# Optimization experiments

Measured on AMD Instinct MI355X. Metric: run time of the kernel, lower is better.

The kernel has to match this reference:

```python
import jax, jax.numpy as jnp
import numpy as np

N_NODES = 50000
N_EDGES = 800000
F_IN = 16
F_OUT = 16
HID = 256


def _glorot(key, shape):
    fan_in, fan_out = shape[0], shape[1]
    lim = np.sqrt(6.0 / (fan_in + fan_out)).astype(np.float32)
    return jax.random.uniform(key, shape, jnp.float32, -lim, lim)


def setup_inputs() -> dict:
    key = jax.random.key(0)
    ks = jax.random.split(key, 12)
    x = jax.random.normal(ks[0], (N_NODES, F_IN), jnp.float32)
    edge_index = jax.random.randint(ks[1], (2, N_EDGES), 0, N_NODES, jnp.int64 if jax.config.jax_enable_x64 else jnp.int32)
    return {
        "x": x,
        "edge_index": edge_index,
        # mlp_pre: Linear(F_IN,HID) -> ReLU -> Linear(HID,HID)
        "pre_w1": _glorot(ks[2], (F_IN, HID)),
        "pre_b1": jnp.zeros((HID,), jnp.float32),
        "pre_w2": _glorot(ks[3], (HID, HID)),
        "pre_b2": jnp.zeros((HID,), jnp.float32),
        # GNCAConv edge transform: W h_j + b
        "conv_w": _glorot(ks[4], (HID, HID)),
        "conv_b": jnp.zeros((HID,), jnp.float32),
        # mlp_post: Linear(2*HID,HID) -> ReLU -> Linear(HID,F_OUT)
        "post_w1": _glorot(ks[5], (2 * HID, HID)),
        "post_b1": jnp.zeros((HID,), jnp.float32),
        "post_w2": _glorot(ks[6], (HID, F_OUT)),
        "post_b2": jnp.zeros((F_OUT,), jnp.float32),
    }


def reference(x, edge_index, pre_w1, pre_b1, pre_w2, pre_b2,
              conv_w, conv_b, post_w1, post_b1, post_w2, post_b2):
    # 1. pre-processing MLP: h_i = MLP_pre(s_i)
    h = jax.nn.relu(x @ pre_w1 + pre_b1) @ pre_w2 + pre_b2  # (N, HID)

    # 2. message passing: h_i || sum_{j in N(i)} ReLU(W h_j + b)
    src, dst = edge_index[0], edge_index[1]
    msg = jax.nn.relu(h[src] @ conv_w + conv_b)  # (E, HID)
    agg = jax.ops.segment_sum(msg, dst, num_segments=h.shape[0])  # (N, HID)
    h = jnp.concatenate([h, agg], axis=-1)  # (N, 2*HID)

    # 3. post-processing MLP + tanh output activation
    out = jax.nn.relu(h @ post_w1 + post_b1) @ post_w2 + post_b2
    return jnp.tanh(out)
```

## Files before the change

kernel.cpp:

```cpp
#include <hip/hip_runtime.h>
#include <hip/hip_bf16.h>

using f16x8 = __attribute__((ext_vector_type(8))) _Float16;
using f32x4 = __attribute__((ext_vector_type(4))) float;
using u16 = unsigned short;

__device__ __forceinline__ u16 f2h(float v) {
    _Float16 h = (_Float16)v;
    u16 r; __builtin_memcpy(&r, &h, 2); return r;
}
__device__ __forceinline__ float h2f(u16 x) {
    _Float16 h; __builtin_memcpy(&h, &x, 2); return (float)h;
}

__device__ __forceinline__ int fsw(int row) { return (row & 3) ^ ((row >> 2) & 3); }
__device__ __forceinline__ int aoff(int row, int kq) {
    return row * 32 + ((kq ^ fsw(row)) * 8);
}

__device__ __forceinline__ void gl16(const u16* g, const u16* l) {
    __builtin_amdgcn_global_load_lds(
        (const __attribute__((address_space(1))) unsigned int*)g,
        (__attribute__((address_space(3))) unsigned int*)l, 16, 0, 0);
}

template<int ACT>
__global__ __launch_bounds__(512, 4)
void mfma_k(const u16* __restrict__ A, int lda,
            const u16* __restrict__ BT,
            const float* __restrict__ bias,
            u16* __restrict__ Ch,
            int ldc, int M, int K) {
    __shared__ u16 As[2][128 * 32];
    __shared__ u16 Bs[2][256 * 32];

    const int tid  = threadIdx.x;
    const int brow = blockIdx.x * 128;
    const int lane = tid & 63;
    const int w    = tid >> 6;
    const int wr = w >> 2, wc = w & 3;
    const int lr = lane & 15, lq = lane >> 4;

    const int rsub = lane >> 2;
    const int s    = lane & 3;
    const int rowA  = w * 16 + rsub;
    const int rowB0 = w * 16 + rsub;
    const int rowB1 = 128 + w * 16 + rsub;
    const u16* gA  = A  + (size_t)(brow + rowA) * lda + (s ^ fsw(rowA))  * 8;
    const u16* gB0 = BT + (size_t)rowB0        * K   + (s ^ fsw(rowB0)) * 8;
    const u16* gB1 = BT + (size_t)rowB1        * K   + (s ^ fsw(rowB1)) * 8;

    f32x4 acc[4][4] = {};

#define STAGE(buf, koff)                                                       \
    do {                                                                       \
        gl16(gA  + (koff), &As[buf][w * 512]);                                 \
        gl16(gB0 + (koff), &Bs[buf][w * 512]);                                 \
        gl16(gB1 + (koff), &Bs[buf][(8 + w) * 512]);                           \
    } while (0)

    STAGE(0, 0);
    __syncthreads();

    const int nt = K >> 5;
    int cur = 0;
    for (int t = 0; t < nt; ++t) {
        if (t + 1 < nt) STAGE(cur ^ 1, (t + 1) * 32);

        f16x8 bf[4];
        #pragma unroll
        for (int n = 0; n < 4; ++n)
            bf[n] = *reinterpret_cast<const f16x8*>(&Bs[cur][aoff(wc * 64 + n * 16 + lr, lq)]);
        #pragma unroll
        for (int m = 0; m < 4; ++m) {
            f16x8 af = *reinterpret_cast<const f16x8*>(&As[cur][aoff(wr * 64 + m * 16 + lr, lq)]);
            #pragma unroll
            for (int n = 0; n < 4; ++n)
                acc[m][n] = __builtin_amdgcn_mfma_f32_16x16x32_f16(af, bf[n], acc[m][n], 0, 0, 0);
        }

        if (t + 1 < nt) {
            __syncthreads();
            cur ^= 1;
        }
    }
#undef STAGE

    #pragma unroll
    for (int m = 0; m < 4; ++m) {
        #pragma unroll
        for (int n = 0; n < 4; ++n) {
            #pragma unroll
            for (int r = 0; r < 4; ++r) {
                int grow = brow + wr * 64 + m * 16 + lq * 4 + r;
                if (grow >= M) continue;
                int gcol = wc * 64 + n * 16 + lr;
                float v = acc[m][n][r] + bias[gcol];
                if (ACT == 1) v = fmaxf(v, 0.f);
                Ch[(size_t)grow * ldc + gcol] = f2h(v);
            }
        }
    }
}

__global__ __launch_bounds__(512, 4)
void mfmaz_k(const u16* __restrict__ A, int lda,
             const u16* __restrict__ BT,
             const float* __restrict__ bias,
             const u16* __restrict__ P2T, const float* __restrict__ b2,
             float* __restrict__ out, int M, int K) {
    __shared__ u16 pool[2 * 128 * 32 + 2 * 256 * 32];
    u16 (*As)[128 * 32] = reinterpret_cast<u16(*)[128 * 32]>(pool);
    u16 (*Bs)[256 * 32] = reinterpret_cast<u16(*)[256 * 32]>(pool + 2 * 128 * 32);
    u16 (*zs)[136]      = reinterpret_cast<u16(*)[136]>(pool);

    const int tid  = threadIdx.x;
    const int brow = blockIdx.x * 128;
    const int lane = tid & 63;
    const int w    = tid >> 6;
    const int wr = w >> 2, wc = w & 3;
    const int lr = lane & 15, lq = lane >> 4;

    const int rsub = lane >> 2;
    const int s    = lane & 3;
    const int rowA  = w * 16 + rsub;
    const int rowB0 = w * 16 + rsub;
    const int rowB1 = 128 + w * 16 + rsub;
    const u16* gA  = A  + (size_t)(brow + rowA) * lda + (s ^ fsw(rowA))  * 8;
    const u16* gB0 = BT + (size_t)rowB0        * K   + (s ^ fsw(rowB0)) * 8;
    const u16* gB1 = BT + (size_t)rowB1        * K   + (s ^ fsw(rowB1)) * 8;

    f32x4 acc[4][4] = {};

#define STAGE(buf, koff)                                                       \
    do {                                                                       \
        gl16(gA  + (koff), &As[buf][w * 512]);                                 \
        gl16(gB0 + (koff), &Bs[buf][w * 512]);                                 \
        gl16(gB1 + (koff), &Bs[buf][(8 + w) * 512]);                           \
    } while (0)

    STAGE(0, 0);
    __syncthreads();

    const int nt = K >> 5;
    int cur = 0;
    for (int t = 0; t < nt; ++t) {
        if (t + 1 < nt) STAGE(cur ^ 1, (t + 1) * 32);

        f16x8 bf[4];
        #pragma unroll
        for (int n = 0; n < 4; ++n)
            bf[n] = *reinterpret_cast<const f16x8*>(&Bs[cur][aoff(wc * 64 + n * 16 + lr, lq)]);
        #pragma unroll
        for (int m = 0; m < 4; ++m) {
            f16x8 af = *reinterpret_cast<const f16x8*>(&As[cur][aoff(wr * 64 + m * 16 + lr, lq)]);
            #pragma unroll
            for (int n = 0; n < 4; ++n)
                acc[m][n] = __builtin_amdgcn_mfma_f32_16x16x32_f16(af, bf[n], acc[m][n], 0, 0, 0);
        }

        if (t + 1 < nt) {
            __syncthreads();
            cur ^= 1;
        }
    }
#undef STAGE

    __syncthreads();

    f32x4 acc2 = {};
    #pragma unroll
    for (int p = 0; p < 2; ++p) {
        if ((wc >> 1) == p) {
            const int colp = (wc & 1) * 64;
            #pragma unroll
            for (int m = 0; m < 4; ++m) {
                #pragma unroll
                for (int n = 0; n < 4; ++n) {
                    #pragma unroll
                    for (int r = 0; r < 4; ++r) {
                        int row  = wr * 64 + m * 16 + lq * 4 + r;
                        int gcol = wc * 64 + n * 16 + lr;
                        float v = fmaxf(acc[m][n][r] + bias[gcol], 0.f);
                        zs[row][colp + n * 16 + lr] = f2h(v);
                    }
                }
            }
        }
        __syncthreads();
        #pragma unroll
        for (int ks = 0; ks < 4; ++ks) {
            f16x8 af = *reinterpret_cast<const f16x8*>(&zs[w * 16 + lr][ks * 32 + lq * 8]);
            f16x8 bf = *reinterpret_cast<const f16x8*>(P2T + lr * 256 + p * 128 + ks * 32 + lq * 8);
            acc2 = __builtin_amdgcn_mfma_f32_16x16x32_f16(af, bf, acc2, 0, 0, 0);
        }
        __syncthreads();
    }

    const float b = b2[lr];
    #pragma unroll
    for (int r = 0; r < 4; ++r) {
        int grow = brow + w * 16 + lq * 4 + r;
        if (grow < M) out[(size_t)grow * 16 + lr] = tanhf(acc2[r] + b);
    }
}

__global__ __launch_bounds__(256)
void setup_k(const float* __restrict__ pre_w2, const float* __restrict__ pre_b2,
             const float* __restrict__ conv_w, const float* __restrict__ conv_b,
             const float* __restrict__ post_w1, const float* __restrict__ post_b1,
             const float* __restrict__ post_w2,
             const float* __restrict__ x, const float* __restrict__ pre_w1,
             const float* __restrict__ pre_b1,
             u16* __restrict__ wcT, float* __restrict__ btc,
             u16* __restrict__ zWT, float* __restrict__ bzc,
             u16* __restrict__ p2T, int* __restrict__ counts,
             u16* __restrict__ t0, int nsb, int N) {
    const int b = blockIdx.x;
    const int n = threadIdx.x;
    if (b < 514) {
        const bool second = (b >= 257);
        const int k = second ? (b - 257) : b;
        const float* B    = second ? post_w1 : conv_w;
        const float* addv = second ? post_b1 : conv_b;
        u16*  WT   = second ? zWT : wcT;
        float* bo  = second ? bzc : btc;
        const int ldout = second ? 512 : 256;
        __shared__ float a_sh[256];
        const bool isBias = (k == 256);
        a_sh[n] = isBias ? pre_b2[n] : pre_w2[(size_t)k * 256 + n];
        __syncthreads();
        float s = 0.f;
        #pragma unroll 8
        for (int j = 0; j < 256; ++j)
            s = fmaf(a_sh[j], B[(size_t)j * 256 + n], s);
        if (isBias) bo[n] = s + addv[n];
        else        WT[(size_t)n * ldout + k] = f2h(s);
    } else if (b < 770) {
        const int j = b - 514;
        zWT[(size_t)j * 512 + 256 + n] = f2h(post_w1[(size_t)(256 + n) * 256 + j]);
    } else if (b < 786) {
        const int j = b - 770;
        p2T[(size_t)j * 256 + n] = f2h(post_w2[(size_t)n * 16 + j]);
    } else if (b < 786 + nsb) {
        const int i = (b - 786) * 256 + n;
        if (i < N) counts[i] = 0;
    } else {
        __shared__ float ws[16 * 256];
        __shared__ float xs[16][17];
        const int r0 = (b - 786 - nsb) * 16;
        for (int i = n; i < 16 * 256; i += 256) ws[i] = pre_w1[i];
        {
            int rr = n >> 4, cc = n & 15;
            xs[rr][cc] = (r0 + rr < N) ? x[(size_t)(r0 + rr) * 16 + cc] : 0.f;
        }
        __syncthreads();
        const float bb = pre_b1[n];
        for (int r = 0; r < 16; r++) {
            if (r0 + r >= N) break;
            float acc = bb;
            #pragma unroll
            for (int k = 0; k < 16; k++) acc = fmaf(xs[r][k], ws[k * 256 + n], acc);
            t0[(size_t)(r0 + r) * 512 + n] = f2h(fmaxf(acc, 0.f));
        }
    }
}

__global__ void hist_k(const int* __restrict__ dst, int E,
                       int* __restrict__ counts, int* __restrict__ rank) {
    int i = blockIdx.x * blockDim.x + threadIdx.x;
    if (i < E) rank[i] = atomicAdd(&counts[dst[i]], 1);
}

__global__ __launch_bounds__(256)
void scan1_k(const int* __restrict__ counts, int* __restrict__ pre,
             int* __restrict__ bsum, int n) {
    __shared__ int sh[256];
    const int t = threadIdx.x;
    const int i = blockIdx.x * 256 + t;
    int v = (i < n) ? counts[i] : 0;
    sh[t] = v;
    __syncthreads();
    #pragma unroll
    for (int d = 1; d < 256; d <<= 1) {
        int x = (t >= d) ? sh[t - d] : 0;
        __syncthreads();
        sh[t] += x;
        __syncthreads();
    }
    if (i < n) pre[i] = sh[t] - v;
    if (t == 255) bsum[blockIdx.x] = sh[255];
}

__global__ __launch_bounds__(256)
void scan3_k(const int* __restrict__ pre, const int* __restrict__ bsum,
             int* __restrict__ offsets, int n, int nb, int total) {
    __shared__ int sh[256];
    const int t = threadIdx.x;
    const int bid = blockIdx.x;
    sh[t] = (t < nb && t < bid) ? bsum[t] : 0;
    __syncthreads();
    #pragma unroll
    for (int d = 128; d > 0; d >>= 1) {
        if (t < d) sh[t] += sh[t + d];
        __syncthreads();
    }
    const int boff = sh[0];
    const int i = bid * 256 + t;
    if (i < n) offsets[i] = pre[i] + boff;
    if (i == 0) offsets[n] = total;
}

__global__ void fill_k(const int* __restrict__ src, const int* __restrict__ dst,
                       const int* __restrict__ rank, int E,
                       const int* __restrict__ offsets, int* __restrict__ sorted_src) {
    int i = blockIdx.x * blockDim.x + threadIdx.x;
    if (i < E) sorted_src[offsets[dst[i]] + rank[i]] = src[i];
}

__global__ void agg_k(const u16* __restrict__ t, const int* __restrict__ offsets,
                      const int* __restrict__ sorted_src,
                      u16* __restrict__ out, int n) {
    const int node = blockIdx.x * (blockDim.x >> 6) + (threadIdx.x >> 6);
    const int lane = threadIdx.x & 63;
    if (node >= n) return;
    const int s0 = offsets[node], s1 = offsets[node + 1];

    float4 a0 = make_float4(0.f, 0.f, 0.f, 0.f);
    float4 a1 = a0, a2 = a0, a3 = a0;

    int i = s0;
    for (; i + 8 <= s1; i += 8) {
        int e0 = sorted_src[i];
        int e1 = sorted_src[i + 1];
        int e2 = sorted_src[i + 2];
        int e3 = sorted_src[i + 3];
        int e4 = sorted_src[i + 4];
        int e5 = sorted_src[i + 5];
        int e6 = sorted_src[i + 6];
        int e7 = sorted_src[i + 7];
        ushort4 v0 = *reinterpret_cast<const ushort4*>(t + (size_t)e0 * 256 + lane * 4);
        ushort4 v1 = *reinterpret_cast<const ushort4*>(t + (size_t)e1 * 256 + lane * 4);
        ushort4 v2 = *reinterpret_cast<const ushort4*>(t + (size_t)e2 * 256 + lane * 4);
        ushort4 v3 = *reinterpret_cast<const ushort4*>(t + (size_t)e3 * 256 + lane * 4);
        ushort4 v4 = *reinterpret_cast<const ushort4*>(t + (size_t)e4 * 256 + lane * 4);
        ushort4 v5 = *reinterpret_cast<const ushort4*>(t + (size_t)e5 * 256 + lane * 4);
        ushort4 v6 = *reinterpret_cast<const ushort4*>(t + (size_t)e6 * 256 + lane * 4);
        ushort4 v7 = *reinterpret_cast<const ushort4*>(t + (size_t)e7 * 256 + lane * 4);
        a0.x += h2f(v0.x); a0.y += h2f(v0.y); a0.z += h2f(v0.z); a0.w += h2f(v0.w);
        a1.x += h2f(v1.x); a1.y += h2f(v1.y); a1.z += h2f(v1.z); a1.w += h2f(v1.w);
        a2.x += h2f(v2.x); a2.y += h2f(v2.y); a2.z += h2f(v2.z); a2.w += h2f(v2.w);
        a3.x += h2f(v3.x); a3.y += h2f(v3.y); a3.z += h2f(v3.z); a3.w += h2f(v3.w);
        a0.x += h2f(v4.x); a0.y += h2f(v4.y); a0.z += h2f(v4.z); a0.w += h2f(v4.w);
        a1.x += h2f(v5.x); a1.y += h2f(v5.y); a1.z += h2f(v5.z); a1.w += h2f(v5.w);
        a2.x += h2f(v6.x); a2.y += h2f(v6.y); a2.z += h2f(v6.z); a2.w += h2f(v6.w);
        a3.x += h2f(v7.x); a3.y += h2f(v7.y); a3.z += h2f(v7.z); a3.w += h2f(v7.w);
    }
    for (; i + 4 <= s1; i += 4) {
        int e0 = sorted_src[i];
        int e1 = sorted_src[i + 1];
        int e2 = sorted_src[i + 2];
        int e3 = sorted_src[i + 3];
        ushort4 v0 = *reinterpret_cast<const ushort4*>(t + (size_t)e0 * 256 + lane * 4);
        ushort4 v1 = *reinterpret_cast<const ushort4*>(t + (size_t)e1 * 256 + lane * 4);
        ushort4 v2 = *reinterpret_cast<const ushort4*>(t + (size_t)e2 * 256 + lane * 4);
        ushort4 v3 = *reinterpret_cast<const ushort4*>(t + (size_t)e3 * 256 + lane * 4);
        a0.x += h2f(v0.x); a0.y += h2f(v0.y); a0.z += h2f(v0.z); a0.w += h2f(v0.w);
        a1.x += h2f(v1.x); a1.y += h2f(v1.y); a1.z += h2f(v1.z); a1.w += h2f(v1.w);
        a2.x += h2f(v2.x); a2.y += h2f(v2.y); a2.z += h2f(v2.z); a2.w += h2f(v2.w);
        a3.x += h2f(v3.x); a3.y += h2f(v3.y); a3.z += h2f(v3.z); a3.w += h2f(v3.w);
    }
    for (; i < s1; ++i) {
        int e0 = sorted_src[i];
        ushort4 v0 = *reinterpret_cast<const ushort4*>(t + (size_t)e0 * 256 + lane * 4);
        a0.x += h2f(v0.x); a0.y += h2f(v0.y); a0.z += h2f(v0.z); a0.w += h2f(v0.w);
    }
    float4 acc;
    acc.x = (a0.x + a1.x) + (a2.x + a3.x);
    acc.y = (a0.y + a1.y) + (a2.y + a3.y);
    acc.z = (a0.z + a1.z) + (a2.z + a3.z);
    acc.w = (a0.w + a1.w) + (a2.w + a3.w);

    ushort4 h4;
    h4.x = f2h(acc.x); h4.y = f2h(acc.y); h4.z = f2h(acc.z); h4.w = f2h(acc.w);
    *reinterpret_cast<ushort4*>(out + (size_t)node * 512 + 256 + (size_t)lane * 4) = h4;
}

extern "C" void kernel_launch(void* const* d_in, const int* in_sizes, int n_in,
                              void* d_out, int out_size, void* d_ws, size_t ws_size,
                              hipStream_t stream) {
    const float* x       = (const float*)d_in[0];
    const int*   edges   = (const int*)d_in[1];
    const float* pre_w1  = (const float*)d_in[2];
    const float* pre_b1  = (const float*)d_in[3];
    const float* pre_w2  = (const float*)d_in[4];
    const float* pre_b2  = (const float*)d_in[5];
    const float* conv_w  = (const float*)d_in[6];
    const float* conv_b  = (const float*)d_in[7];
    const float* post_w1 = (const float*)d_in[8];
    const float* post_b1 = (const float*)d_in[9];
    const float* post_w2 = (const float*)d_in[10];
    const float* post_b2 = (const float*)d_in[11];

    const int N = in_sizes[0] / 16;
    const int E = in_sizes[1] / 2;
    const int* src = edges;
    const int* dst = edges + E;

    const int Mp128 = (N + 127) & ~127;

    u16*   hcat = (u16*)d_ws;
    u16*   tf16 = hcat + (size_t)Mp128 * 512;
    u16*   wcT  = tf16 + (size_t)Mp128 * 256;
    u16*   zWT  = wcT + 256 * 256;
    u16*   p2T  = zWT + 256 * 512;
    float* btc  = (float*)(p2T + 16 * 256);
    float* bzc  = btc + 256;
    int* offsets = (int*)(bzc + 256);
    int* counts  = offsets + (N + 1);
    int* rank    = counts + N;
    int* sorted  = rank + E;
    int* pre     = sorted + E;
    int* bsum    = pre + N;

    const dim3 blk(256);
    const int nsb = (N + 255) / 256;
    const int npre = (N + 15) / 16;

    setup_k<<<786 + nsb + npre, blk, 0, stream>>>(
        pre_w2, pre_b2, conv_w, conv_b, post_w1, post_b1, post_w2,
        x, pre_w1, pre_b1,
        wcT, btc, zWT, bzc, p2T, counts, hcat, nsb, N);

    hist_k<<<(E + 255) / 256, blk, 0, stream>>>(dst, E, counts, rank);
    scan1_k<<<nsb, blk, 0, stream>>>(counts, pre, bsum, N);
    scan3_k<<<nsb, blk, 0, stream>>>(pre, bsum, offsets, N, nsb, E);
    fill_k<<<(E + 255) / 256, blk, 0, stream>>>(src, dst, rank, E, offsets, sorted);

    mfma_k<1><<<Mp128 / 128, dim3(512), 0, stream>>>(hcat, 512, wcT, btc,
                                                     tf16, 256, N, 256);
    agg_k<<<(N + 3) / 4, blk, 0, stream>>>(tf16, offsets, sorted, hcat, N);
    mfmaz_k<<<Mp128 / 128, dim3(512), 0, stream>>>(hcat, 512, zWT, bzc,
                                                   p2T, post_b2, (float*)d_out, N, 512);
}
```

Baseline: 178.5 us.

## Fuse histogram into setup kernel and CSR fill into message GEMM

The edge histogram (atomic rank assignment) moves into extra blocks of the setup kernel, and the counts array is zeroed with a memset before it. The CSR fill step runs as extra blocks appended to the message GEMM kernel, so the fill overlaps the GEMM and two kernel launches go away. The risk is that the fill blocks reserve the GEMM's large shared-memory footprint and 512-thread shape, which may reduce occupancy for those lightweight blocks.

```diff
diff --git a/kernel.cpp b/kernel.cpp
--- a/kernel.cpp
+++ b/kernel.cpp
@@ -24,15 +24,23 @@
         (__attribute__((address_space(3))) unsigned int*)l, 16, 0, 0);
 }
 
-template<int ACT>
 __global__ __launch_bounds__(512, 4)
-void mfma_k(const u16* __restrict__ A, int lda,
-            const u16* __restrict__ BT,
-            const float* __restrict__ bias,
-            u16* __restrict__ Ch,
-            int ldc, int M, int K) {
+void gemmfill_k(const u16* __restrict__ A, int lda,
+                const u16* __restrict__ BT,
+                const float* __restrict__ bias,
+                u16* __restrict__ Ch,
+                int ldc, int M, int K, int NT,
+                const int* __restrict__ esrc, const int* __restrict__ edst,
+                const int* __restrict__ rank, const int* __restrict__ offsets,
+                int* __restrict__ sorted, int E) {
     __shared__ u16 As[2][128 * 32];
     __shared__ u16 Bs[2][256 * 32];
+
+    if (blockIdx.x >= NT) {
+        int i = (blockIdx.x - NT) * 512 + threadIdx.x;
+        if (i < E) sorted[offsets[edst[i]] + rank[i]] = esrc[i];
+        return;
+    }
 
     const int tid  = threadIdx.x;
     const int brow = blockIdx.x * 128;
@@ -95,8 +103,7 @@
                 int grow = brow + wr * 64 + m * 16 + lq * 4 + r;
                 if (grow >= M) continue;
                 int gcol = wc * 64 + n * 16 + lr;
-                float v = acc[m][n][r] + bias[gcol];
-                if (ACT == 1) v = fmaxf(v, 0.f);
+                float v = fmaxf(acc[m][n][r] + bias[gcol], 0.f);
                 Ch[(size_t)grow * ldc + gcol] = f2h(v);
             }
         }
@@ -212,10 +219,12 @@
              const float* __restrict__ post_w2,
              const float* __restrict__ x, const float* __restrict__ pre_w1,
              const float* __restrict__ pre_b1,
+             const int* __restrict__ edst,
              u16* __restrict__ wcT, float* __restrict__ btc,
              u16* __restrict__ zWT, float* __restrict__ bzc,
              u16* __restrict__ p2T, int* __restrict__ counts,
-             u16* __restrict__ t0, int nsb, int N) {
+             int* __restrict__ rank,
+             u16* __restrict__ t0, int npre, int N, int E) {
     const int b = blockIdx.x;
     const int n = threadIdx.x;
     if (b < 514) {
@@ -242,13 +251,10 @@
     } else if (b < 786) {
         const int j = b - 770;
         p2T[(size_t)j * 256 + n] = f2h(post_w2[(size_t)n * 16 + j]);
-    } else if (b < 786 + nsb) {
-        const int i = (b - 786) * 256 + n;
-        if (i < N) counts[i] = 0;
-    } else {
+    } else if (b < 786 + npre) {
         __shared__ float ws[16 * 256];
         __shared__ float xs[16][17];
-        const int r0 = (b - 786 - nsb) * 16;
+        const int r0 = (b - 786) * 16;
         for (int i = n; i < 16 * 256; i += 256) ws[i] = pre_w1[i];
         {
             int rr = n >> 4, cc = n & 15;
@@ -263,13 +269,10 @@
             for (int k = 0; k < 16; k++) acc = fmaf(xs[r][k], ws[k * 256 + n], acc);
             t0[(size_t)(r0 + r) * 512 + n] = f2h(fmaxf(acc, 0.f));
         }
-    }
-}
-
-__global__ void hist_k(const int* __restrict__ dst, int E,
-                       int* __restrict__ counts, int* __restrict__ rank) {
-    int i = blockIdx.x * blockDim.x + threadIdx.x;
-    if (i < E) rank[i] = atomicAdd(&counts[dst[i]], 1);
+    } else {
+        const int i = (b - 786 - npre) * 256 + n;
+        if (i < E) rank[i] = atomicAdd(&counts[edst[i]], 1);
+    }
 }
 
 __global__ __launch_bounds__(256)
@@ -309,13 +312,6 @@
     const int i = bid * 256 + t;
     if (i < n) offsets[i] = pre[i] + boff;
     if (i == 0) offsets[n] = total;
-}
-
-__global__ void fill_k(const int* __restrict__ src, const int* __restrict__ dst,
-                       const int* __restrict__ rank, int E,
-                       const int* __restrict__ offsets, int* __restrict__ sorted_src) {
-    int i = blockIdx.x * blockDim.x + threadIdx.x;
-    if (i < E) sorted_src[offsets[dst[i]] + rank[i]] = src[i];
 }
 
 __global__ void agg_k(const u16* __restrict__ t, const int* __restrict__ offsets,
@@ -424,22 +420,27 @@
     int* bsum    = pre + N;
 
     const dim3 blk(256);
-    const int nsb = (N + 255) / 256;
-    const int npre = (N + 15) / 16;
-
-    setup_k<<<786 + nsb + npre, blk, 0, stream>>>(
+    const int nsb   = (N + 255) / 256;
+    const int npre  = (N + 15) / 16;
+    const int nhist = (E + 255) / 256;
+    const int NT    = Mp128 / 128;
+    const int nfill = (E + 511) / 512;
+
+    hipMemsetAsync(counts, 0, (size_t)N * sizeof(int), stream);
+    setup_k<<<786 + npre + nhist, blk, 0, stream>>>(
         pre_w2, pre_b2, conv_w, conv_b, post_w1, post_b1, post_w2,
-        x, pre_w1, pre_b1,
-        wcT, btc, zWT, bzc, p2T, counts, hcat, nsb, N);
-
-    hist_k<<<(E + 255) / 256, blk, 0, stream>>>(dst, E, counts, rank);
+        x, pre_w1, pre_b1, dst,
+        wcT, btc, zWT, bzc, p2T, counts, rank, hcat, npre, N, E);
+
     scan1_k<<<nsb, blk, 0, stream>>>(counts, pre, bsum, N);
     scan3_k<<<nsb, blk, 0, stream>>>(pre, bsum, offsets, N, nsb, E);
-    fill_k<<<(E + 255) / 256, blk, 0, stream>>>(src, dst, rank, E, offsets, sorted);
-
-    mfma_k<1><<<Mp128 / 128, dim3(512), 0, stream>>>(hcat, 512, wcT, btc,
-                                                     tf16, 256, N, 256);
+
+    gemmfill_k<<<NT + nfill, dim3(512), 0, stream>>>(
+        hcat, 512, wcT, btc, tf16, 256, N, 256, NT,
+        src, dst, rank, offsets, sorted, E);
+
     agg_k<<<(N + 3) / 4, blk, 0, stream>>>(tf16, offsets, sorted, hcat, N);
+
     mfmaz_k<<<Mp128 / 128, dim3(512), 0, stream>>>(hcat, 512, zWT, bzc,
                                                    p2T, post_b2, (float*)d_out, N, 512);
 }
```

Result: slower. 198.6 us (+11.3%).
